# Kernel optimization log

Measured on AMD Instinct MI355X. Metric: run time of the kernel, lower is better.

Reference implementation:

```python
import jax, jax.numpy as jnp
import numpy as np

B, M, C = 8, 1024, 768


def setup_inputs() -> dict:
    key = jax.random.key(0)
    ks = jax.random.split(key, 10)
    s = 0.02
    return {
        "layout_x": jax.random.normal(ks[0], (B, M, C), jnp.float32),
        "text_x": jax.random.normal(ks[1], (B, M, C), jnp.float32),
        "mask": jax.random.randint(ks[2], (B, M), 0, 2).astype(jnp.float32),
        "Wqkv": jax.random.normal(ks[3], (C, 3 * C), jnp.float32) * s,
        "bqkv": jnp.zeros((3 * C,), jnp.float32),
        "Wq": jax.random.normal(ks[4], (C, C), jnp.float32) * s,
        "bq": jnp.zeros((C,), jnp.float32),
        "Wkv": jax.random.normal(ks[5], (C, 2 * C), jnp.float32) * s,
        "bkv": jnp.zeros((2 * C,), jnp.float32),
        "Wffn": jax.random.normal(ks[6], (C, C), jnp.float32) * s,
        "bffn": jnp.zeros((C,), jnp.float32),
    }


def _masked_attn(q, k, v, pair_mask, scale):
    # pair_mask: [B,M,M] True where valid (mask_i * mask_j != 0)
    scores = jnp.einsum("bmd,bnd->bmn", q, k) * scale  # [B,M,M]
    scores = jnp.where(pair_mask, scores, jnp.float32(-10000.0))
    attn = jax.nn.softmax(scores, axis=-1)
    return jnp.einsum("bmn,bnd->bmd", attn, v)


def reference(layout_x, text_x, mask, Wqkv, bqkv, Wq, bq, Wkv, bkv, Wffn, bffn):
    dim = layout_x.shape[-1]
    scale = dim ** (-0.5)
    # mask repeated over C then mask@mask.T / C  ==  outer product of 1D masks
    pair = (mask[:, :, None] * mask[:, None, :]) != 0  # [B,M,M] bool, True=keep

    # self-attention on layout_x
    qkv = layout_x @ Wqkv + bqkv  # [B,M,3C]
    q, k, v = jnp.split(qkv, 3, axis=-1)
    layout_o = _masked_attn(q, k, v, pair, scale)

    # cross-attention: q from layout output, k/v from text_x
    cq = layout_o @ Wq + bq
    kv = text_x @ Wkv + bkv  # [B,M,2C]
    ck, cv = jnp.split(kv, 2, axis=-1)
    merge = _masked_attn(cq, ck, cv, pair, scale)

    return merge @ Wffn + bffn
```

## Files before the change

kernel.cpp:

```cpp
#include <hip/hip_runtime.h>
#include <math.h>

#define BDIM 8
#define MDIM 1024
#define CDIM 768
#define ROWS (BDIM * MDIM)

typedef __attribute__((ext_vector_type(8))) short short8;
typedef __attribute__((ext_vector_type(8))) unsigned short ushort8;
typedef __attribute__((ext_vector_type(4))) float f32x4;

#define MFMA16(a, b, c) __builtin_amdgcn_mfma_f32_16x16x32_bf16((a), (b), (c), 0, 0, 0)

__device__ __forceinline__ unsigned short f2bf(float f) {
  unsigned u = __float_as_uint(f);
  return (unsigned short)((u + 0x7FFFu + ((u >> 16) & 1u)) >> 16);
}

__global__ __launch_bounds__(256) void prologue(
    const float* __restrict__ xl, const float* __restrict__ xt,
    unsigned short* __restrict__ dxl, unsigned short* __restrict__ dxt,
    const float* __restrict__ W0, const float* __restrict__ W1,
    const float* __restrict__ W2, const float* __restrict__ W3,
    unsigned short* __restrict__ D0, unsigned short* __restrict__ D1,
    unsigned short* __restrict__ D2, unsigned short* __restrict__ D3,
    float* __restrict__ rowsum) {
  const int bx = blockIdx.x;
  const int tid = threadIdx.x;
  if (bx < 6144) {
    const float* src = bx < 3072 ? xl : xt;
    unsigned short* dst = bx < 3072 ? dxl : dxt;
    const int i = ((bx < 3072 ? bx : bx - 3072) * 256 + tid) * 8;
    const float4 a = *(const float4*)(src + i);
    const float4 b = *(const float4*)(src + i + 4);
    ushort8 o;
    o[0] = f2bf(a.x); o[1] = f2bf(a.y); o[2] = f2bf(a.z); o[3] = f2bf(a.w);
    o[4] = f2bf(b.x); o[5] = f2bf(b.y); o[6] = f2bf(b.z); o[7] = f2bf(b.w);
    *(ushort8*)(dst + i) = o;
  } else if (bx < 6152) {
    const int i = ((bx - 6144) * 256 + tid) * 8;
    const float4 z = {0.f, 0.f, 0.f, 0.f};
    *(float4*)(rowsum + i) = z;
    *(float4*)(rowsum + i + 4) = z;
  } else {
    int x = bx - 6152;
    int bxx = x % 168;
    const int k0 = (x / 168) * 32;
    const float* W; unsigned short* D; int N;
    if (bxx < 72)       { W = W0; D = D0; N = 2304; }
    else if (bxx < 96)  { W = W1; D = D1; N = 768;  bxx -= 72; }
    else if (bxx < 144) { W = W2; D = D2; N = 1536; bxx -= 96; }
    else                { W = W3; D = D3; N = 768;  bxx -= 144; }
    __shared__ unsigned short t[32][33];
    const int tx = tid & 31, ty = tid >> 5;
    const int n0 = bxx * 32;
#pragma unroll
    for (int i = 0; i < 4; ++i)
      t[ty + i * 8][tx] = f2bf(W[(size_t)(k0 + ty + i * 8) * N + n0 + tx]);
    __syncthreads();
#pragma unroll
    for (int i = 0; i < 4; ++i)
      D[(size_t)(n0 + ty + i * 8) * CDIM + k0 + tx] = t[tx][ty + i * 8];
  }
}

__device__ __forceinline__ void stage64(
    const unsigned short* __restrict__ g, int ld, int k0,
    unsigned short* lds, int wave, int lane) {
  const int gchunk = (lane & 7) ^ (lane >> 3);
#pragma unroll
  for (int j = 0; j < 4; ++j) {
    const int grp = wave * 4 + j;
    const unsigned short* gp =
        g + (size_t)(grp * 8 + (lane >> 3)) * ld + k0 + gchunk * 8;
    __builtin_amdgcn_global_load_lds(
        (const __attribute__((address_space(1))) unsigned int*)gp,
        (__attribute__((address_space(3))) unsigned int*)(lds + grp * 512),
        16, 0, 0);
  }
}

__device__ __forceinline__ void mfma_loop64(
    const unsigned short* __restrict__ A, int lda,
    const unsigned short* __restrict__ Bt, int ldb, int K,
    unsigned short* As, unsigned short* Bs, f32x4 acc[4][4],
    int wave, int lane) {
  const int wx = wave & 1, wy = wave >> 1;
  const int quad = lane >> 4, l16 = lane & 15;
  for (int k0 = 0; k0 < K; k0 += 64) {
    stage64(A, lda, k0, As, wave, lane);
    stage64(Bt, ldb, k0, Bs, wave, lane);
    __syncthreads();
#pragma unroll
    for (int h = 0; h < 2; ++h) {
      const int slot = ((((h << 2) | quad) ^ (l16 & 7))) * 8;
      short8 afr[4], bfr[4];
#pragma unroll
      for (int mt = 0; mt < 4; ++mt)
        afr[mt] = *(const short8*)&As[(wy * 64 + mt * 16 + l16) * 64 + slot];
#pragma unroll
      for (int nt = 0; nt < 4; ++nt)
        bfr[nt] = *(const short8*)&Bs[(wx * 64 + nt * 16 + l16) * 64 + slot];
#pragma unroll
      for (int mt = 0; mt < 4; ++mt)
#pragma unroll
        for (int nt = 0; nt < 4; ++nt)
          acc[mt][nt] = MFMA16(afr[mt], bfr[nt], acc[mt][nt]);
    }
    __syncthreads();
  }
}

__device__ __forceinline__ void proj_epilogue(
    f32x4 acc[4][4], const float* __restrict__ bias,
    unsigned short* __restrict__ Y, unsigned short* __restrict__ vTd,
    int c0, int m0, int lastSlice, int trans, int wave, int lane) {
  const int wx = wave & 1, wy = wave >> 1;
  const int quad = lane >> 4, l16 = lane & 15;
  const int slice = c0 / 768;
  if (trans && slice == lastSlice) {
#pragma unroll
    for (int mt = 0; mt < 4; ++mt) {
      const int row0 = m0 + wy * 64 + mt * 16 + quad * 4;
      const int b = row0 >> 10, n0 = row0 & 1023;
#pragma unroll
      for (int nt = 0; nt < 4; ++nt) {
        const int gcol = c0 + wx * 64 + nt * 16 + l16;
        const int d = gcol - slice * 768;
        const float bv = bias[gcol];
        uint2 o;
        o.x = (unsigned)f2bf(acc[mt][nt][0] + bv) |
              ((unsigned)f2bf(acc[mt][nt][1] + bv) << 16);
        o.y = (unsigned)f2bf(acc[mt][nt][2] + bv) |
              ((unsigned)f2bf(acc[mt][nt][3] + bv) << 16);
        *(uint2*)&vTd[((size_t)b * CDIM + d) * MDIM + n0] = o;
      }
    }
  } else {
    const size_t sbase = (size_t)slice * ROWS * 768;
#pragma unroll
    for (int mt = 0; mt < 4; ++mt)
#pragma unroll
      for (int nt = 0; nt < 4; ++nt) {
        const int gcol = c0 + wx * 64 + nt * 16 + l16;
        const int lcol = gcol - slice * 768;
        const float bv = bias[gcol];
#pragma unroll
        for (int rg = 0; rg < 4; ++rg) {
          const int row = m0 + wy * 64 + mt * 16 + quad * 4 + rg;
          Y[sbase + (size_t)row * 768 + lcol] = f2bf(acc[mt][nt][rg] + bv);
        }
      }
  }
}

__device__ __forceinline__ void swizzle_mc(int lin, int* m0, int* c0) {
  const int xcd = lin & 7, j = lin >> 3;
  *m0 = (xcd * 8 + (j & 7)) * 128;
  *c0 = (j >> 3) * 128;
}

__global__ __launch_bounds__(256, 4) void gemm_proj(
    const unsigned short* __restrict__ A, const unsigned short* __restrict__ Bt,
    const float* __restrict__ bias, unsigned short* __restrict__ Y,
    unsigned short* __restrict__ vTd, int trans) {
  __shared__ __align__(16) unsigned short As[128 * 64];
  __shared__ __align__(16) unsigned short Bs[128 * 64];
  int m0, c0;
  swizzle_mc(blockIdx.y * gridDim.x + blockIdx.x, &m0, &c0);
  const int tid = threadIdx.x;
  const int wave = tid >> 6, lane = tid & 63;
  const f32x4 vzero = {0.f, 0.f, 0.f, 0.f};
  f32x4 acc[4][4];
#pragma unroll
  for (int mt = 0; mt < 4; ++mt)
#pragma unroll
    for (int nt = 0; nt < 4; ++nt) acc[mt][nt] = vzero;
  mfma_loop64(A + (size_t)m0 * CDIM, CDIM, Bt + (size_t)c0 * CDIM, CDIM, CDIM,
              As, Bs, acc, wave, lane);
  proj_epilogue(acc, bias, Y, vTd, c0, m0, (int)(gridDim.x / 6) - 1, trans,
                wave, lane);
}

__global__ __launch_bounds__(256, 4) void gemm_proj_dual(
    const unsigned short* __restrict__ A0, const unsigned short* __restrict__ B0,
    const float* __restrict__ b0, unsigned short* __restrict__ Y0,
    const unsigned short* __restrict__ A1, const unsigned short* __restrict__ B1,
    const float* __restrict__ b1, unsigned short* __restrict__ Y1,
    unsigned short* __restrict__ vTd) {
  __shared__ __align__(16) unsigned short As[128 * 64];
  __shared__ __align__(16) unsigned short Bs[128 * 64];
  int lin = blockIdx.x;
  const unsigned short *A, *Bt;
  const float* bias;
  unsigned short* Y;
  int gx, trans;
  if (lin < 384) { A = A0; Bt = B0; bias = b0; Y = Y0; gx = 6;  trans = 0; }
  else { lin -= 384; A = A1; Bt = B1; bias = b1; Y = Y1; gx = 12; trans = 1; }
  int m0, c0;
  swizzle_mc(lin, &m0, &c0);
  const int tid = threadIdx.x;
  const int wave = tid >> 6, lane = tid & 63;
  const f32x4 vzero = {0.f, 0.f, 0.f, 0.f};
  f32x4 acc[4][4];
#pragma unroll
  for (int mt = 0; mt < 4; ++mt)
#pragma unroll
    for (int nt = 0; nt < 4; ++nt) acc[mt][nt] = vzero;
  mfma_loop64(A + (size_t)m0 * CDIM, CDIM, Bt + (size_t)c0 * CDIM, CDIM, CDIM,
              As, Bs, acc, wave, lane);
  proj_epilogue(acc, bias, Y, vTd, c0, m0, gx / 6 - 1, trans, wave, lane);
}

__global__ __launch_bounds__(256, 4) void gemm_ffn(
    const unsigned short* __restrict__ A, const unsigned short* __restrict__ Bt,
    const float* __restrict__ bias, float* __restrict__ Y) {
  __shared__ __align__(16) unsigned short As[128 * 64];
  __shared__ __align__(16) unsigned short Bs[128 * 64];
  int m0, c0;
  swizzle_mc(blockIdx.y * gridDim.x + blockIdx.x, &m0, &c0);
  const int tid = threadIdx.x;
  const int wave = tid >> 6, lane = tid & 63;
  const int wx = wave & 1, wy = wave >> 1;
  const int quad = lane >> 4, l16 = lane & 15;
  const f32x4 vzero = {0.f, 0.f, 0.f, 0.f};
  f32x4 acc[4][4];
#pragma unroll
  for (int mt = 0; mt < 4; ++mt)
#pragma unroll
    for (int nt = 0; nt < 4; ++nt) acc[mt][nt] = vzero;
  mfma_loop64(A + (size_t)m0 * CDIM, CDIM, Bt + (size_t)c0 * CDIM, CDIM, CDIM,
              As, Bs, acc, wave, lane);
#pragma unroll
  for (int mt = 0; mt < 4; ++mt)
#pragma unroll
    for (int nt = 0; nt < 4; ++nt) {
      const int col = c0 + wx * 64 + nt * 16 + l16;
      const float bv = bias[col];
#pragma unroll
      for (int rg = 0; rg < 4; ++rg) {
        const int row = m0 + wy * 64 + mt * 16 + quad * 4 + rg;
        Y[(size_t)row * 768 + col] = acc[mt][nt][rg] + bv;
      }
    }
}

__global__ __launch_bounds__(256, 4) void gemm_qk(
    const unsigned short* __restrict__ Qb, const unsigned short* __restrict__ Kb,
    const float* __restrict__ mask, unsigned short* __restrict__ S, float scale,
    float* __restrict__ rowsum) {
  __shared__ __align__(16) unsigned short As[128 * 64];
  __shared__ __align__(16) unsigned short Bs[128 * 64];
  const int c0 = blockIdx.x * 128;
  const int m0 = blockIdx.y * 128;
  const int b = blockIdx.z;
  const int tid = threadIdx.x;
  const int wave = tid >> 6, lane = tid & 63;
  const int wx = wave & 1, wy = wave >> 1;
  const int quad = lane >> 4, l16 = lane & 15;

  const f32x4 vzero = {0.f, 0.f, 0.f, 0.f};
  f32x4 acc[4][4];
#pragma unroll
  for (int mt = 0; mt < 4; ++mt)
#pragma unroll
    for (int nt = 0; nt < 4; ++nt) acc[mt][nt] = vzero;

  mfma_loop64(Qb + ((size_t)b * MDIM + m0) * CDIM, CDIM,
              Kb + ((size_t)b * MDIM + c0) * CDIM, CDIM, CDIM,
              As, Bs, acc, wave, lane);

  const float* maskb = mask + b * MDIM;
  float mrow[4][4], rsum[4][4];
#pragma unroll
  for (int mt = 0; mt < 4; ++mt)
#pragma unroll
    for (int rg = 0; rg < 4; ++rg) {
      mrow[mt][rg] = maskb[m0 + wy * 64 + mt * 16 + quad * 4 + rg];
      rsum[mt][rg] = 0.f;
    }
  unsigned short* Sb = S + (size_t)b * MDIM * MDIM;
#pragma unroll
  for (int nt = 0; nt < 4; ++nt) {
    const int col = c0 + wx * 64 + nt * 16 + l16;
    const float mcol = maskb[col];
#pragma unroll
    for (int mt = 0; mt < 4; ++mt)
#pragma unroll
      for (int rg = 0; rg < 4; ++rg) {
        const int row = m0 + wy * 64 + mt * 16 + quad * 4 + rg;
        const float e = (mrow[mt][rg] * mcol != 0.f)
                            ? __expf(acc[mt][nt][rg] * scale)
                            : 1e-30f;
        Sb[(size_t)row * MDIM + col] = f2bf(e);
        rsum[mt][rg] += e;
      }
  }
  for (int off = 1; off < 16; off <<= 1) {
#pragma unroll
    for (int mt = 0; mt < 4; ++mt)
#pragma unroll
      for (int rg = 0; rg < 4; ++rg)
        rsum[mt][rg] += __shfl_xor(rsum[mt][rg], off, 64);
  }
  if (l16 == 0) {
    float* rsb = rowsum + (b << 10) + m0 + wy * 64;
#pragma unroll
    for (int mt = 0; mt < 4; ++mt)
#pragma unroll
      for (int rg = 0; rg < 4; ++rg)
        atomicAdd(&rsb[mt * 16 + quad * 4 + rg], rsum[mt][rg]);
  }
}

__global__ __launch_bounds__(256, 4) void attn_pv(
    const unsigned short* __restrict__ P, const unsigned short* __restrict__ vT,
    unsigned short* __restrict__ O, const float* __restrict__ rowsum) {
  __shared__ __align__(16) unsigned short As[128 * 64];
  __shared__ __align__(16) unsigned short Bs[128 * 64];
  const int c0 = blockIdx.x * 128;
  const int m0 = blockIdx.y * 128;
  const int b = blockIdx.z;
  const int tid = threadIdx.x;
  const int wave = tid >> 6, lane = tid & 63;
  const int wx = wave & 1, wy = wave >> 1;
  const int quad = lane >> 4, l16 = lane & 15;

  const f32x4 vzero = {0.f, 0.f, 0.f, 0.f};
  f32x4 acc[4][4];
#pragma unroll
  for (int mt = 0; mt < 4; ++mt)
#pragma unroll
    for (int nt = 0; nt < 4; ++nt) acc[mt][nt] = vzero;

  mfma_loop64(P + ((size_t)b * MDIM + m0) * MDIM, MDIM,
              vT + ((size_t)b * CDIM + c0) * MDIM, MDIM, MDIM,
              As, Bs, acc, wave, lane);

  const float* rsb = rowsum + (b << 10) + m0 + wy * 64;
  float inv[4][4];
#pragma unroll
  for (int mt = 0; mt < 4; ++mt)
#pragma unroll
    for (int rg = 0; rg < 4; ++rg)
      inv[mt][rg] = 1.f / rsb[mt * 16 + quad * 4 + rg];
#pragma unroll
  for (int mt = 0; mt < 4; ++mt)
#pragma unroll
    for (int nt = 0; nt < 4; ++nt)
#pragma unroll
      for (int rg = 0; rg < 4; ++rg) {
        const int row = m0 + wy * 64 + mt * 16 + quad * 4 + rg;
        const int col = c0 + wx * 64 + nt * 16 + l16;
        O[(size_t)(b * MDIM + row) * CDIM + col] =
            f2bf(acc[mt][nt][rg] * inv[mt][rg]);
      }
}

extern "C" void kernel_launch(void* const* d_in, const int* in_sizes, int n_in,
                              void* d_out, int out_size, void* d_ws, size_t ws_size,
                              hipStream_t stream) {
  const float* layout_x = (const float*)d_in[0];
  const float* text_x   = (const float*)d_in[1];
  const float* maskp    = (const float*)d_in[2];
  const float* Wqkv     = (const float*)d_in[3];
  const float* bqkv     = (const float*)d_in[4];
  const float* Wq       = (const float*)d_in[5];
  const float* bq       = (const float*)d_in[6];
  const float* Wkv      = (const float*)d_in[7];
  const float* bkv      = (const float*)d_in[8];
  const float* Wffn     = (const float*)d_in[9];
  const float* bffn     = (const float*)d_in[10];
  float* out = (float*)d_out;
  char* ws = (char*)d_ws;

  const float scale = 1.0f / sqrtf((float)CDIM);

  unsigned short* xlb    = (unsigned short*)(ws);
  unsigned short* xtb    = (unsigned short*)(ws + 12582912);
  unsigned short* Wqkv_t = (unsigned short*)(ws + 25165824);
  unsigned short* Wq_t   = (unsigned short*)(ws + 28704768);
  unsigned short* Wkv_t  = (unsigned short*)(ws + 29884416);
  unsigned short* Wffn_t = (unsigned short*)(ws + 32243712);
  unsigned short* Qb     = (unsigned short*)(ws + 33423360);
  unsigned short* Kb     = (unsigned short*)(ws + 46006272);
  unsigned short* cqb    = (unsigned short*)(ws + 58589184);
  unsigned short* vT     = (unsigned short*)(ws + 71172096);
  unsigned short* S      = (unsigned short*)(ws + 83755008);
  unsigned short* attn1  = xlb;
  unsigned short* Kc     = Qb;
  float* rowsum1 = out;
  float* rowsum2 = out + 8192;

  prologue<<<10184, 256, 0, stream>>>(layout_x, text_x, xlb, xtb,
                                      Wqkv, Wq, Wkv, Wffn,
                                      Wqkv_t, Wq_t, Wkv_t, Wffn_t, rowsum1);
  gemm_proj<<<dim3(18, 64), 256, 0, stream>>>(xlb, Wqkv_t, bqkv, Qb, vT, 1);
  gemm_qk<<<dim3(8, 8, BDIM), 256, 0, stream>>>(Qb, Kb, maskp, S, scale, rowsum1);
  attn_pv<<<dim3(6, 8, BDIM), 256, 0, stream>>>(S, vT, attn1, rowsum1);
  gemm_proj_dual<<<1152, 256, 0, stream>>>(attn1, Wq_t, bq, cqb,
                                           xtb, Wkv_t, bkv, Kc, vT);
  gemm_qk<<<dim3(8, 8, BDIM), 256, 0, stream>>>(cqb, Kc, maskp, S, scale, rowsum2);
  attn_pv<<<dim3(6, 8, BDIM), 256, 0, stream>>>(S, vT, attn1, rowsum2);
  gemm_ffn<<<dim3(6, 64), 256, 0, stream>>>(attn1, Wffn_t, bffn, out);
}
```

Before: 321.4 us.

## Fuse QKV and text KV projections into one 256x256 pipelined GEMM kernel

```diff
diff --git a/kernel.cpp b/kernel.cpp
--- a/kernel.cpp
+++ b/kernel.cpp
@@ -11,6 +11,12 @@
 typedef __attribute__((ext_vector_type(4))) float f32x4;
 
 #define MFMA16(a, b, c) __builtin_amdgcn_mfma_f32_16x16x32_bf16((a), (b), (c), 0, 0, 0)
+
+#define BAR() __builtin_amdgcn_s_barrier()
+#define FENCE() asm volatile("" ::: "memory")
+#define WAIT_LGKM0() asm volatile("s_waitcnt lgkmcnt(0)" ::: "memory")
+#define WAIT_VM6() asm volatile("s_waitcnt vmcnt(6)" ::: "memory")
+#define WAIT_VM0() asm volatile("s_waitcnt vmcnt(0)" ::: "memory")
 
 __device__ __forceinline__ unsigned short f2bf(float f) {
   unsigned u = __float_as_uint(f);
@@ -23,8 +29,7 @@
     const float* __restrict__ W0, const float* __restrict__ W1,
     const float* __restrict__ W2, const float* __restrict__ W3,
     unsigned short* __restrict__ D0, unsigned short* __restrict__ D1,
-    unsigned short* __restrict__ D2, unsigned short* __restrict__ D3,
-    float* __restrict__ rowsum) {
+    unsigned short* __restrict__ D2, unsigned short* __restrict__ D3) {
   const int bx = blockIdx.x;
   const int tid = threadIdx.x;
   if (bx < 6144) {
@@ -37,13 +42,8 @@
     o[0] = f2bf(a.x); o[1] = f2bf(a.y); o[2] = f2bf(a.z); o[3] = f2bf(a.w);
     o[4] = f2bf(b.x); o[5] = f2bf(b.y); o[6] = f2bf(b.z); o[7] = f2bf(b.w);
     *(ushort8*)(dst + i) = o;
-  } else if (bx < 6152) {
-    const int i = ((bx - 6144) * 256 + tid) * 8;
-    const float4 z = {0.f, 0.f, 0.f, 0.f};
-    *(float4*)(rowsum + i) = z;
-    *(float4*)(rowsum + i + 4) = z;
   } else {
-    int x = bx - 6152;
+    int x = bx - 6144;
     int bxx = x % 168;
     const int k0 = (x / 168) * 32;
     const float* W; unsigned short* D; int N;
@@ -158,6 +158,183 @@
   const int xcd = lin & 7, j = lin >> 3;
   *m0 = (xcd * 8 + (j & 7)) * 128;
   *c0 = (j >> 3) * 128;
+}
+
+__device__ __forceinline__ void stage_half256(
+    const unsigned short* __restrict__ g, int k0,
+    unsigned short* lds, int wave, int lane) {
+  const int gchunk = (lane & 7) ^ (lane >> 3);
+#pragma unroll
+  for (int j = 0; j < 2; ++j) {
+    const int grp = wave * 2 + j;
+    const unsigned short* gp =
+        g + (size_t)(grp * 8 + (lane >> 3)) * CDIM + k0 + gchunk * 8;
+    __builtin_amdgcn_global_load_lds(
+        (const __attribute__((address_space(1))) unsigned int*)gp,
+        (__attribute__((address_space(3))) unsigned int*)(lds + grp * 512),
+        16, 0, 0);
+  }
+}
+
+__device__ __forceinline__ void read_fragsA(
+    const unsigned short* h, int roff, short8 fr[4][2], int l16, int quad) {
+#pragma unroll
+  for (int mf = 0; mf < 4; ++mf)
+#pragma unroll
+    for (int kh = 0; kh < 2; ++kh) {
+      const int slot = (((kh << 2) | quad) ^ (l16 & 7)) * 8;
+      fr[mf][kh] = *(const short8*)&h[(roff + mf * 16 + l16) * 64 + slot];
+    }
+}
+
+__device__ __forceinline__ void read_fragsB(
+    const unsigned short* h, int roff, short8 fr[2][2], int l16, int quad) {
+#pragma unroll
+  for (int nf = 0; nf < 2; ++nf)
+#pragma unroll
+    for (int kh = 0; kh < 2; ++kh) {
+      const int slot = (((kh << 2) | quad) ^ (l16 & 7)) * 8;
+      fr[nf][kh] = *(const short8*)&h[(roff + nf * 16 + l16) * 64 + slot];
+    }
+}
+
+#define MFMA_PHASE(GM, GN, BB)                                              \
+  do {                                                                      \
+    __builtin_amdgcn_s_setprio(1);                                          \
+    _Pragma("unroll") for (int mf = 0; mf < 4; ++mf)                        \
+    _Pragma("unroll") for (int nf = 0; nf < 2; ++nf)                        \
+    _Pragma("unroll") for (int kh = 0; kh < 2; ++kh)                        \
+        acc[GM][GN][mf][nf] =                                               \
+            MFMA16(afr[mf][kh], BB[nf][kh], acc[GM][GN][mf][nf]);           \
+    __builtin_amdgcn_s_setprio(0);                                          \
+  } while (0)
+
+__global__ __launch_bounds__(512, 2) void gemm_qkvkv(
+    const unsigned short* __restrict__ A0g, const unsigned short* __restrict__ B0g,
+    const float* __restrict__ bias0, unsigned short* __restrict__ Y0,
+    unsigned short* __restrict__ vT0,
+    const unsigned short* __restrict__ A1g, const unsigned short* __restrict__ B1g,
+    const float* __restrict__ bias1, unsigned short* __restrict__ Y1,
+    unsigned short* __restrict__ vT1) {
+  __shared__ __align__(16) unsigned short lds[65536];
+  int lin = blockIdx.x;
+  const unsigned short *A, *Bt; const float* bias;
+  unsigned short *Y, *vTd; int lastSlice, m0, c0;
+  if (lin < 288) {
+    A = A0g; Bt = B0g; bias = bias0; Y = Y0; vTd = vT0; lastSlice = 2;
+    const int xcd = lin & 7, j = lin >> 3;
+    m0 = (xcd * 4 + (j & 3)) * 256; c0 = (j >> 2) * 256;
+  } else {
+    lin -= 288;
+    A = A1g; Bt = B1g; bias = bias1; Y = Y1; vTd = vT1; lastSlice = 1;
+    const int xcd = lin & 7, j = lin >> 3;
+    m0 = (xcd * 4 + (j & 3)) * 256; c0 = (j >> 2) * 256;
+  }
+  const int tid = threadIdx.x;
+  const int wave = tid >> 6, lane = tid & 63;
+  const int wy = wave >> 2, wx = wave & 3;
+  const int quad = lane >> 4, l16 = lane & 15;
+
+  const unsigned short* Ah[2] = {A + (size_t)m0 * CDIM,
+                                 A + (size_t)(m0 + 128) * CDIM};
+  const unsigned short* Bh[2] = {Bt + (size_t)c0 * CDIM,
+                                 Bt + (size_t)(c0 + 128) * CDIM};
+
+  const f32x4 vzero = {0.f, 0.f, 0.f, 0.f};
+  f32x4 acc[2][2][4][2];
+#pragma unroll
+  for (int gm = 0; gm < 2; ++gm)
+#pragma unroll
+    for (int gn = 0; gn < 2; ++gn)
+#pragma unroll
+      for (int mf = 0; mf < 4; ++mf)
+#pragma unroll
+        for (int nf = 0; nf < 2; ++nf) acc[gm][gn][mf][nf] = vzero;
+  short8 afr[4][2], b0r[2][2], b1r[2][2];
+
+  stage_half256(Ah[0], 0, lds + 0, wave, lane);
+  stage_half256(Bh[0], 0, lds + 16384, wave, lane);
+  stage_half256(Bh[1], 0, lds + 24576, wave, lane);
+  stage_half256(Ah[1], 0, lds + 8192, wave, lane);
+  stage_half256(Ah[0], 64, lds + 32768 + 0, wave, lane);
+  stage_half256(Bh[0], 64, lds + 32768 + 16384, wave, lane);
+  stage_half256(Bh[1], 64, lds + 32768 + 24576, wave, lane);
+  WAIT_VM6();
+  BAR(); FENCE();
+
+  for (int t = 0; t < 12; ++t) {
+    unsigned short* bufc = lds + (t & 1) * 32768;
+    unsigned short* bufn = lds + ((t + 1) & 1) * 32768;
+    read_fragsA(bufc + 0, wy * 64, afr, l16, quad);
+    read_fragsB(bufc + 16384, wx * 32, b0r, l16, quad);
+    if (t < 11) stage_half256(Ah[1], (t + 1) * 64, bufn + 8192, wave, lane);
+    BAR(); WAIT_LGKM0();
+    MFMA_PHASE(0, 0, b0r);
+    BAR(); FENCE();
+    read_fragsB(bufc + 24576, wx * 32, b1r, l16, quad);
+    if (t < 10) stage_half256(Ah[0], (t + 2) * 64, bufc + 0, wave, lane);
+    BAR(); WAIT_LGKM0();
+    MFMA_PHASE(0, 1, b1r);
+    BAR(); FENCE();
+    read_fragsA(bufc + 8192, wy * 64, afr, l16, quad);
+    if (t < 10) stage_half256(Bh[0], (t + 2) * 64, bufc + 16384, wave, lane);
+    BAR(); WAIT_LGKM0();
+    MFMA_PHASE(1, 0, b0r);
+    BAR(); FENCE();
+    if (t < 10) {
+      stage_half256(Bh[1], (t + 2) * 64, bufc + 24576, wave, lane);
+      WAIT_VM6();
+    } else if (t == 10) {
+      WAIT_VM0();
+    }
+    BAR(); WAIT_LGKM0();
+    MFMA_PHASE(1, 1, b1r);
+    BAR(); FENCE();
+  }
+
+#pragma unroll
+  for (int gm = 0; gm < 2; ++gm)
+#pragma unroll
+    for (int gn = 0; gn < 2; ++gn) {
+      const int cb2 = c0 + gn * 128 + wx * 32;
+      const int slice = cb2 / 768;
+      const int rb = m0 + gm * 128 + wy * 64;
+      if (slice == lastSlice) {
+#pragma unroll
+        for (int mf = 0; mf < 4; ++mf) {
+          const int row0 = rb + mf * 16 + quad * 4;
+          const int b = row0 >> 10, n0 = row0 & 1023;
+#pragma unroll
+          for (int nf = 0; nf < 2; ++nf) {
+            const int gcol = cb2 + nf * 16 + l16;
+            const int d = gcol - slice * 768;
+            const float bv = bias[gcol];
+            uint2 o;
+            o.x = (unsigned)f2bf(acc[gm][gn][mf][nf][0] + bv) |
+                  ((unsigned)f2bf(acc[gm][gn][mf][nf][1] + bv) << 16);
+            o.y = (unsigned)f2bf(acc[gm][gn][mf][nf][2] + bv) |
+                  ((unsigned)f2bf(acc[gm][gn][mf][nf][3] + bv) << 16);
+            *(uint2*)&vTd[((size_t)b * CDIM + d) * MDIM + n0] = o;
+          }
+        }
+      } else {
+        const size_t sbase = (size_t)slice * ROWS * 768;
+#pragma unroll
+        for (int mf = 0; mf < 4; ++mf)
+#pragma unroll
+          for (int nf = 0; nf < 2; ++nf) {
+            const int gcol = cb2 + nf * 16 + l16;
+            const int lcol = gcol - slice * 768;
+            const float bv = bias[gcol];
+#pragma unroll
+            for (int rg = 0; rg < 4; ++rg) {
+              const int row = rb + mf * 16 + quad * 4 + rg;
+              Y[sbase + (size_t)row * 768 + lcol] =
+                  f2bf(acc[gm][gn][mf][nf][rg] + bv);
+            }
+          }
+      }
+    }
 }
 
 __global__ __launch_bounds__(256, 4) void gemm_proj(
@@ -180,36 +357,6 @@
               As, Bs, acc, wave, lane);
   proj_epilogue(acc, bias, Y, vTd, c0, m0, (int)(gridDim.x / 6) - 1, trans,
                 wave, lane);
-}
-
-__global__ __launch_bounds__(256, 4) void gemm_proj_dual(
-    const unsigned short* __restrict__ A0, const unsigned short* __restrict__ B0,
-    const float* __restrict__ b0, unsigned short* __restrict__ Y0,
-    const unsigned short* __restrict__ A1, const unsigned short* __restrict__ B1,
-    const float* __restrict__ b1, unsigned short* __restrict__ Y1,
-    unsigned short* __restrict__ vTd) {
-  __shared__ __align__(16) unsigned short As[128 * 64];
-  __shared__ __align__(16) unsigned short Bs[128 * 64];
-  int lin = blockIdx.x;
-  const unsigned short *A, *Bt;
-  const float* bias;
-  unsigned short* Y;
-  int gx, trans;
-  if (lin < 384) { A = A0; Bt = B0; bias = b0; Y = Y0; gx = 6;  trans = 0; }
-  else { lin -= 384; A = A1; Bt = B1; bias = b1; Y = Y1; gx = 12; trans = 1; }
-  int m0, c0;
-  swizzle_mc(lin, &m0, &c0);
-  const int tid = threadIdx.x;
-  const int wave = tid >> 6, lane = tid & 63;
-  const f32x4 vzero = {0.f, 0.f, 0.f, 0.f};
-  f32x4 acc[4][4];
-#pragma unroll
-  for (int mt = 0; mt < 4; ++mt)
-#pragma unroll
-    for (int nt = 0; nt < 4; ++nt) acc[mt][nt] = vzero;
-  mfma_loop64(A + (size_t)m0 * CDIM, CDIM, Bt + (size_t)c0 * CDIM, CDIM, CDIM,
-              As, Bs, acc, wave, lane);
-  proj_epilogue(acc, bias, Y, vTd, c0, m0, gx / 6 - 1, trans, wave, lane);
 }
 
 __global__ __launch_bounds__(256, 4) void gemm_ffn(
@@ -248,7 +395,7 @@
 __global__ __launch_bounds__(256, 4) void gemm_qk(
     const unsigned short* __restrict__ Qb, const unsigned short* __restrict__ Kb,
     const float* __restrict__ mask, unsigned short* __restrict__ S, float scale,
-    float* __restrict__ rowsum) {
+    float* __restrict__ rsp) {
   __shared__ __align__(16) unsigned short As[128 * 64];
   __shared__ __align__(16) unsigned short Bs[128 * 64];
   const int c0 = blockIdx.x * 128;
@@ -304,18 +451,19 @@
         rsum[mt][rg] += __shfl_xor(rsum[mt][rg], off, 64);
   }
   if (l16 == 0) {
-    float* rsb = rowsum + (b << 10) + m0 + wy * 64;
+    float* rs = rsp + ((((size_t)blockIdx.x * 2 + wx) * 8 + b) << 10) +
+                m0 + wy * 64;
 #pragma unroll
     for (int mt = 0; mt < 4; ++mt)
 #pragma unroll
       for (int rg = 0; rg < 4; ++rg)
-        atomicAdd(&rsb[mt * 16 + quad * 4 + rg], rsum[mt][rg]);
+        rs[mt * 16 + quad * 4 + rg] = rsum[mt][rg];
   }
 }
 
 __global__ __launch_bounds__(256, 4) void attn_pv(
     const unsigned short* __restrict__ P, const unsigned short* __restrict__ vT,
-    unsigned short* __restrict__ O, const float* __restrict__ rowsum) {
+    unsigned short* __restrict__ O, const float* __restrict__ rsp) {
   __shared__ __align__(16) unsigned short As[128 * 64];
   __shared__ __align__(16) unsigned short Bs[128 * 64];
   const int c0 = blockIdx.x * 128;
@@ -337,13 +485,16 @@
               vT + ((size_t)b * CDIM + c0) * MDIM, MDIM, MDIM,
               As, Bs, acc, wave, lane);
 
-  const float* rsb = rowsum + (b << 10) + m0 + wy * 64;
+  const float* rsb = rsp + (((size_t)l16 * 8 + b) << 10) + m0 + wy * 64;
   float inv[4][4];
 #pragma unroll
   for (int mt = 0; mt < 4; ++mt)
 #pragma unroll
-    for (int rg = 0; rg < 4; ++rg)
-      inv[mt][rg] = 1.f / rsb[mt * 16 + quad * 4 + rg];
+    for (int rg = 0; rg < 4; ++rg) {
+      float s = rsb[mt * 16 + quad * 4 + rg];
+      for (int off = 1; off < 16; off <<= 1) s += __shfl_xor(s, off, 64);
+      inv[mt][rg] = 1.f / s;
+    }
 #pragma unroll
   for (int mt = 0; mt < 4; ++mt)
 #pragma unroll
@@ -388,19 +539,19 @@
   unsigned short* vT     = (unsigned short*)(ws + 71172096);
   unsigned short* S      = (unsigned short*)(ws + 83755008);
   unsigned short* attn1  = xlb;
-  unsigned short* Kc     = Qb;
-  float* rowsum1 = out;
-  float* rowsum2 = out + 8192;
-
-  prologue<<<10184, 256, 0, stream>>>(layout_x, text_x, xlb, xtb,
+  unsigned short* cK  = (unsigned short*)out;
+  unsigned short* cVT = (unsigned short*)out + 6291456;
+  float* rsp = (float*)xtb;
+
+  prologue<<<10176, 256, 0, stream>>>(layout_x, text_x, xlb, xtb,
                                       Wqkv, Wq, Wkv, Wffn,
-                                      Wqkv_t, Wq_t, Wkv_t, Wffn_t, rowsum1);
-  gemm_proj<<<dim3(18, 64), 256, 0, stream>>>(xlb, Wqkv_t, bqkv, Qb, vT, 1);
-  gemm_qk<<<dim3(8, 8, BDIM), 256, 0, stream>>>(Qb, Kb, maskp, S, scale, rowsum1);
-  attn_pv<<<dim3(6, 8, BDIM), 256, 0, stream>>>(S, vT, attn1, rowsum1);
-  gemm_proj_dual<<<1152, 256, 0, stream>>>(attn1, Wq_t, bq, cqb,
-                                           xtb, Wkv_t, bkv, Kc, vT);
-  gemm_qk<<<dim3(8, 8, BDIM), 256, 0, stream>>>(cqb, Kc, maskp, S, scale, rowsum2);
-  attn_pv<<<dim3(6, 8, BDIM), 256, 0, stream>>>(S, vT, attn1, rowsum2);
+                                      Wqkv_t, Wq_t, Wkv_t, Wffn_t);
+  gemm_qkvkv<<<480, 512, 0, stream>>>(xlb, Wqkv_t, bqkv, Qb, vT,
+                                      xtb, Wkv_t, bkv, cK, cVT);
+  gemm_qk<<<dim3(8, 8, BDIM), 256, 0, stream>>>(Qb, Kb, maskp, S, scale, rsp);
+  attn_pv<<<dim3(6, 8, BDIM), 256, 0, stream>>>(S, vT, attn1, rsp);
+  gemm_proj<<<dim3(6, 64), 256, 0, stream>>>(attn1, Wq_t, bq, cqb, vT, 0);
+  gemm_qk<<<dim3(8, 8, BDIM), 256, 0, stream>>>(cqb, cK, maskp, S, scale, rsp);
+  attn_pv<<<dim3(6, 8, BDIM), 256, 0, stream>>>(S, cVT, attn1, rsp);
   gemm_ffn<<<dim3(6, 64), 256, 0, stream>>>(attn1, Wffn_t, bffn, out);
 }
```

Result: faster. 314.3 us (-2.2%).
